# Kernel tuning notes

Hardware: AMD Instinct MI355X
Metric: run time of the kernel (lower is better)

Reference implementation:

```python
import jax, jax.numpy as jnp
import numpy as np

MARGIN = 1.0
EPS = 1e-8  # torch.cosine_similarity default eps


def _cosine(a, b):
    num = jnp.sum(a * b, axis=1)
    den = jnp.maximum(jnp.linalg.norm(a, axis=1) * jnp.linalg.norm(b, axis=1), EPS)
    return num / den


def setup_inputs() -> dict:
    key = jax.random.key(0)
    k1, k2 = jax.random.split(key)
    B, D = 8192, 512
    anchor = jax.random.normal(k1, (B, D), dtype=jnp.float32)
    positive = jax.random.normal(k2, (B, D), dtype=jnp.float32)
    return {"anchor": anchor, "positive": positive}


def reference(anchor, positive):
    B = positive.shape[0]
    a_n = anchor / jnp.linalg.norm(anchor, axis=1, keepdims=True)
    p_n = positive / jnp.linalg.norm(positive, axis=1, keepdims=True)
    sim = a_n @ p_n.T                      # [B, B] cosine similarity
    mask = 1.0 - jnp.eye(B, dtype=sim.dtype)
    sim = sim * mask                       # zero diagonal
    # margin branch of NegariveSampler (margin=1): abs(sim - margin), zeros -> -inf, argmax
    score = jnp.abs(sim - MARGIN) * mask
    score = jnp.where(score == 0.0, -jnp.inf, score)
    neg_idx = jnp.argmax(score, axis=1)    # [B]
    neg = p_n[neg_idx]                     # gather normalized positives as negatives
    cos_ap = _cosine(anchor, positive)
    cos_an = _cosine(anchor, neg)
    loss = jax.nn.relu(MARGIN + cos_ap - cos_an)
    return loss.mean()
```

## Files before the change

kernel.cpp:

```cpp
#include <hip/hip_runtime.h>
#include <stdint.h>

typedef int   i32x8 __attribute__((ext_vector_type(8)));
typedef float f32x4 __attribute__((ext_vector_type(4)));

#define B_ROWS 8192
#define D_DIM  512

__device__ __forceinline__ uint32_t enc_f32(float f) {
  uint32_t s = __float_as_uint(f);
  return (s & 0x80000000u) ? ~s : (s | 0x80000000u);
}
__device__ __forceinline__ float dec_f32(uint32_t e) {
  uint32_t s = (e & 0x80000000u) ? (e ^ 0x80000000u) : ~e;
  return __uint_as_float(s);
}

__global__ __launch_bounds__(256) void norm_kernel(
    const float* __restrict__ anchor, const float* __restrict__ positive,
    uint32_t* __restrict__ a8, uint32_t* __restrict__ p8,
    float* __restrict__ cos_ap, uint32_t* __restrict__ minenc)
{
  const int wave = threadIdx.x >> 6, lane = threadIdx.x & 63;
  const int r = blockIdx.x * 4 + wave;

  const float4* av = (const float4*)(anchor   + (size_t)r * D_DIM) + lane * 2;
  const float4* pv = (const float4*)(positive + (size_t)r * D_DIM) + lane * 2;
  float4 a0 = av[0], a1 = av[1];
  float4 p0 = pv[0], p1 = pv[1];

  float sa = a0.x*a0.x + a0.y*a0.y + a0.z*a0.z + a0.w*a0.w
           + a1.x*a1.x + a1.y*a1.y + a1.z*a1.z + a1.w*a1.w;
  float sp = p0.x*p0.x + p0.y*p0.y + p0.z*p0.z + p0.w*p0.w
           + p1.x*p1.x + p1.y*p1.y + p1.z*p1.z + p1.w*p1.w;
  float dp = a0.x*p0.x + a0.y*p0.y + a0.z*p0.z + a0.w*p0.w
           + a1.x*p1.x + a1.y*p1.y + a1.z*p1.z + a1.w*p1.w;

#pragma unroll
  for (int d = 1; d < 64; d <<= 1) {
    sa += __shfl_xor(sa, d);
    sp += __shfl_xor(sp, d);
    dp += __shfl_xor(dp, d);
  }

  const float na = sqrtf(sa), np = sqrtf(sp);
  const float ia = 1.0f / na, ip = 1.0f / np;

  float na0 = a0.x*ia, na1 = a0.y*ia, na2 = a0.z*ia, na3 = a0.w*ia;
  float na4 = a1.x*ia, na5 = a1.y*ia, na6 = a1.z*ia, na7 = a1.w*ia;
  float np0 = p0.x*ip, np1 = p0.y*ip, np2 = p0.z*ip, np3 = p0.w*ip;
  float np4 = p1.x*ip, np5 = p1.y*ip, np6 = p1.z*ip, np7 = p1.w*ip;

  uint32_t aw0 = __builtin_amdgcn_cvt_pk_fp8_f32(na0, na1, 0,  false);
  aw0          = __builtin_amdgcn_cvt_pk_fp8_f32(na2, na3, aw0, true);
  uint32_t aw1 = __builtin_amdgcn_cvt_pk_fp8_f32(na4, na5, 0,  false);
  aw1          = __builtin_amdgcn_cvt_pk_fp8_f32(na6, na7, aw1, true);
  uint32_t pw0 = __builtin_amdgcn_cvt_pk_fp8_f32(np0, np1, 0,  false);
  pw0          = __builtin_amdgcn_cvt_pk_fp8_f32(np2, np3, pw0, true);
  uint32_t pw1 = __builtin_amdgcn_cvt_pk_fp8_f32(np4, np5, 0,  false);
  pw1          = __builtin_amdgcn_cvt_pk_fp8_f32(np6, np7, pw1, true);

  ((uint2*)a8)[(size_t)r * 64 + lane] = make_uint2(aw0, aw1);
  ((uint2*)p8)[(size_t)r * 64 + lane] = make_uint2(pw0, pw1);

  if (lane == 0) {
    cos_ap[r] = dp / fmaxf(na * np, 1e-8f);
    minenc[r] = 0xFFFFFFFFu;
  }
}

__device__ __forceinline__ void load16_to_lds(const void* g, void* l) {
  __builtin_amdgcn_global_load_lds(
      (__attribute__((address_space(1))) uint32_t*)(uintptr_t)(g),
      (__attribute__((address_space(3))) uint32_t*)(uintptr_t)(l),
      16, 0, 0);
}

__global__ __launch_bounds__(256, 3) void simmin_kernel(
    const uint8_t* __restrict__ a8, const uint8_t* __restrict__ p8,
    uint32_t* __restrict__ minenc)
{
  __shared__ __attribute__((aligned(16))) uint8_t Plds[2][128 * 128];
  __shared__ float redmin[256];

  const int tid  = threadIdx.x;
  const int lane = tid & 63;
  const int wave = tid >> 6;
  const int waveM = wave >> 1, waveN = wave & 1;
  const int quad = lane >> 4;
  const int l15  = lane & 15;

  const int bid = blockIdx.x;
  const int blockRow = (bid & 7) * 8 + ((bid >> 3) & 7);
  const int blockCol = bid >> 6;

  f32x4 acc[4][4];
  const f32x4 zero = {0.f, 0.f, 0.f, 0.f};
#pragma unroll
  for (int i = 0; i < 4; i++)
#pragma unroll
    for (int j = 0; j < 4; j++) acc[i][j] = zero;

  const int srow = lane >> 3;
  const int sk   = (lane & 7) ^ srow;
  const uint8_t* pBase = p8 + (size_t)(blockCol * 128) * D_DIM;

  auto stage = [&](int k0, int buf) {
#pragma unroll
    for (int c = 0; c < 4; c++) {
      const int chunk = wave * 4 + c;
      const size_t goff = (size_t)(chunk * 8 + srow) * D_DIM + k0 + sk * 16;
      load16_to_lds(pBase + goff, &Plds[buf][chunk * 1024]);
    }
  };

  const uint8_t* aFragBase =
      a8 + (size_t)(blockRow * 128 + waveM * 64 + l15) * D_DIM + quad * 32;

  stage(0, 0);

#pragma unroll
  for (int k = 0; k < 4; k++) {
    const int buf = k & 1;
    const int k0  = k * 128;

    i32x8 af[4];
#pragma unroll
    for (int mf = 0; mf < 4; mf++) {
      const uint8_t* ap = aFragBase + (size_t)(mf * 16) * D_DIM + k0;
      const int4 lo = *(const int4*)(ap);
      const int4 hi = *(const int4*)(ap + 16);
      af[mf] = (i32x8){lo.x, lo.y, lo.z, lo.w, hi.x, hi.y, hi.z, hi.w};
    }

    __syncthreads();

    i32x8 bfr[4];
#pragma unroll
    for (int nf = 0; nf < 4; nf++) {
      const int r = waveN * 64 + nf * 16 + l15;
      const int rx = r & 7;
      const int4 lo = *(const int4*)&Plds[buf][r * 128 + (((quad * 2 + 0) ^ rx) * 16)];
      const int4 hi = *(const int4*)&Plds[buf][r * 128 + (((quad * 2 + 1) ^ rx) * 16)];
      bfr[nf] = (i32x8){lo.x, lo.y, lo.z, lo.w, hi.x, hi.y, hi.z, hi.w};
    }

    if (k < 3) stage(k0 + 128, buf ^ 1);

#pragma unroll
    for (int mf = 0; mf < 4; mf++)
#pragma unroll
      for (int nf = 0; nf < 4; nf++)
        acc[mf][nf] = __builtin_amdgcn_mfma_scale_f32_16x16x128_f8f6f4(
            af[mf], bfr[nf], acc[mf][nf],
            0, 0,
            0, 0x7F7F7F7F,
            0, 0x7F7F7F7F);
  }

  const int rowTileBase = blockRow * 128 + waveM * 64;
  const int colTileBase = blockCol * 128 + waveN * 64;

  float rm[4][4];
#pragma unroll
  for (int mf = 0; mf < 4; mf++)
#pragma unroll
    for (int r = 0; r < 4; r++) rm[mf][r] = 3.0e38f;

#pragma unroll
  for (int mf = 0; mf < 4; mf++) {
#pragma unroll
    for (int nf = 0; nf < 4; nf++) {
      const int col = colTileBase + nf * 16 + l15;
#pragma unroll
      for (int r = 0; r < 4; r++) {
        const int row = rowTileBase + mf * 16 + quad * 4 + r;
        const float v = acc[mf][nf][r];
        rm[mf][r] = (row == col) ? rm[mf][r] : fminf(rm[mf][r], v);
      }
    }
  }
#pragma unroll
  for (int d = 1; d < 16; d <<= 1)
#pragma unroll
    for (int mf = 0; mf < 4; mf++)
#pragma unroll
      for (int r = 0; r < 4; r++)
        rm[mf][r] = fminf(rm[mf][r], __shfl_xor(rm[mf][r], d));

  if (l15 == 0) {
#pragma unroll
    for (int mf = 0; mf < 4; mf++)
#pragma unroll
      for (int r = 0; r < 4; r++)
        redmin[waveN * 128 + waveM * 64 + mf * 16 + quad * 4 + r] = rm[mf][r];
  }
  __syncthreads();

  if (tid < 128) {
    const float m = fminf(redmin[tid], redmin[128 + tid]);
    atomicMin(&minenc[blockRow * 128 + tid], enc_f32(m));
  }
}

__global__ __launch_bounds__(1024) void finalize_kernel(
    const uint32_t* __restrict__ minenc, const float* __restrict__ cos_ap,
    float* __restrict__ out)
{
  float sum = 0.0f;
#pragma unroll
  for (int r = threadIdx.x; r < B_ROWS; r += 1024)
    sum += fmaxf(0.0f, 1.0f + cos_ap[r] - dec_f32(minenc[r]));

#pragma unroll
  for (int d = 1; d < 64; d <<= 1) sum += __shfl_xor(sum, d);
  __shared__ float s[16];
  if ((threadIdx.x & 63) == 0) s[threadIdx.x >> 6] = sum;
  __syncthreads();
  if (threadIdx.x < 64) {
    float t = (threadIdx.x < 16) ? s[threadIdx.x] : 0.0f;
#pragma unroll
    for (int d = 1; d < 16; d <<= 1) t += __shfl_xor(t, d);
    if (threadIdx.x == 0) out[0] = t * (1.0f / (float)B_ROWS);
  }
}

extern "C" void kernel_launch(void* const* d_in, const int* in_sizes, int n_in,
                              void* d_out, int out_size, void* d_ws, size_t ws_size,
                              hipStream_t stream) {
  const float* anchor   = (const float*)d_in[0];
  const float* positive = (const float*)d_in[1];

  char* ws = (char*)d_ws;
  uint32_t* a8     = (uint32_t*)(ws);
  uint32_t* p8     = (uint32_t*)(ws + (4ull << 20));
  float*    cos_ap = (float*)(ws + (8ull << 20));
  uint32_t* minenc = (uint32_t*)(ws + (8ull << 20) + (32ull << 10));
  float*    out = (float*)d_out;

  norm_kernel<<<B_ROWS / 4, 256, 0, stream>>>(anchor, positive, a8, p8,
                                              cos_ap, minenc);
  simmin_kernel<<<4096, 256, 0, stream>>>((const uint8_t*)a8,
                                          (const uint8_t*)p8, minenc);
  finalize_kernel<<<1, 1024, 0, stream>>>(minenc, cos_ap, out);
}
```

Before: 152.2 us.

## Fuse finalize reduction into simmin via last-block counter, preload A fragments

Removes the separate finalize kernel launch by having the last simmin block to finish (found with an atomic done counter reset in norm_kernel) run the loss reduction. All four K-slices of A fragments are now loaded into registers up front instead of once per iteration, and launch bounds drop from 3 to 2 blocks per SM so the larger register footprint fits. The aim is to save one launch plus its gap and to hide global load latency, at the cost of occupancy and an extra atomic and fence in every block.

```diff
diff --git a/kernel.cpp b/kernel.cpp
--- a/kernel.cpp
+++ b/kernel.cpp
@@ -6,6 +6,7 @@
 
 #define B_ROWS 8192
 #define D_DIM  512
+#define N_BLOCKS 4096
 
 __device__ __forceinline__ uint32_t enc_f32(float f) {
   uint32_t s = __float_as_uint(f);
@@ -19,10 +20,13 @@
 __global__ __launch_bounds__(256) void norm_kernel(
     const float* __restrict__ anchor, const float* __restrict__ positive,
     uint32_t* __restrict__ a8, uint32_t* __restrict__ p8,
-    float* __restrict__ cos_ap, uint32_t* __restrict__ minenc)
+    float* __restrict__ cos_ap, uint32_t* __restrict__ minenc,
+    uint32_t* __restrict__ donecnt)
 {
   const int wave = threadIdx.x >> 6, lane = threadIdx.x & 63;
   const int r = blockIdx.x * 4 + wave;
+
+  if (blockIdx.x == 0 && threadIdx.x == 0) *donecnt = 0u;
 
   const float4* av = (const float4*)(anchor   + (size_t)r * D_DIM) + lane * 2;
   const float4* pv = (const float4*)(positive + (size_t)r * D_DIM) + lane * 2;
@@ -76,9 +80,10 @@
       16, 0, 0);
 }
 
-__global__ __launch_bounds__(256, 3) void simmin_kernel(
+__global__ __launch_bounds__(256, 2) void simmin_kernel(
     const uint8_t* __restrict__ a8, const uint8_t* __restrict__ p8,
-    uint32_t* __restrict__ minenc)
+    uint32_t* __restrict__ minenc, const float* __restrict__ cos_ap,
+    uint32_t* __restrict__ donecnt, float* __restrict__ out)
 {
   __shared__ __attribute__((aligned(16))) uint8_t Plds[2][128 * 128];
   __shared__ float redmin[256];
@@ -117,21 +122,23 @@
   const uint8_t* aFragBase =
       a8 + (size_t)(blockRow * 128 + waveM * 64 + l15) * D_DIM + quad * 32;
 
+  i32x8 afk[4][4];
+#pragma unroll
+  for (int k = 0; k < 4; k++) {
+#pragma unroll
+    for (int mf = 0; mf < 4; mf++) {
+      const uint8_t* ap = aFragBase + (size_t)(mf * 16) * D_DIM + k * 128;
+      const int4 lo = *(const int4*)(ap);
+      const int4 hi = *(const int4*)(ap + 16);
+      afk[k][mf] = (i32x8){lo.x, lo.y, lo.z, lo.w, hi.x, hi.y, hi.z, hi.w};
+    }
+  }
+
   stage(0, 0);
 
 #pragma unroll
   for (int k = 0; k < 4; k++) {
     const int buf = k & 1;
-    const int k0  = k * 128;
-
-    i32x8 af[4];
-#pragma unroll
-    for (int mf = 0; mf < 4; mf++) {
-      const uint8_t* ap = aFragBase + (size_t)(mf * 16) * D_DIM + k0;
-      const int4 lo = *(const int4*)(ap);
-      const int4 hi = *(const int4*)(ap + 16);
-      af[mf] = (i32x8){lo.x, lo.y, lo.z, lo.w, hi.x, hi.y, hi.z, hi.w};
-    }
 
     __syncthreads();
 
@@ -145,14 +152,14 @@
       bfr[nf] = (i32x8){lo.x, lo.y, lo.z, lo.w, hi.x, hi.y, hi.z, hi.w};
     }
 
-    if (k < 3) stage(k0 + 128, buf ^ 1);
+    if (k < 3) stage((k + 1) * 128, buf ^ 1);
 
 #pragma unroll
     for (int mf = 0; mf < 4; mf++)
 #pragma unroll
       for (int nf = 0; nf < 4; nf++)
         acc[mf][nf] = __builtin_amdgcn_mfma_scale_f32_16x16x128_f8f6f4(
-            af[mf], bfr[nf], acc[mf][nf],
+            afk[k][mf], bfr[nf], acc[mf][nf],
             0, 0,
             0, 0x7F7F7F7F,
             0, 0x7F7F7F7F);
@@ -201,27 +208,33 @@
     const float m = fminf(redmin[tid], redmin[128 + tid]);
     atomicMin(&minenc[blockRow * 128 + tid], enc_f32(m));
   }
-}
-
-__global__ __launch_bounds__(1024) void finalize_kernel(
-    const uint32_t* __restrict__ minenc, const float* __restrict__ cos_ap,
-    float* __restrict__ out)
-{
+
+  __threadfence();
+  __syncthreads();
+  __shared__ int lastFlag;
+  if (tid == 0) {
+    uint32_t prev = __hip_atomic_fetch_add(donecnt, 1u, __ATOMIC_ACQ_REL,
+                                           __HIP_MEMORY_SCOPE_AGENT);
+    lastFlag = (prev == N_BLOCKS - 1);
+  }
+  __syncthreads();
+  if (!lastFlag) return;
+
   float sum = 0.0f;
 #pragma unroll
-  for (int r = threadIdx.x; r < B_ROWS; r += 1024)
-    sum += fmaxf(0.0f, 1.0f + cos_ap[r] - dec_f32(minenc[r]));
-
+  for (int i = 0; i < B_ROWS / 256; i++) {
+    const int r = i * 256 + tid;
+    const uint32_t e = __hip_atomic_load(&minenc[r], __ATOMIC_RELAXED,
+                                         __HIP_MEMORY_SCOPE_AGENT);
+    sum += fmaxf(0.0f, 1.0f + cos_ap[r] - dec_f32(e));
+  }
 #pragma unroll
   for (int d = 1; d < 64; d <<= 1) sum += __shfl_xor(sum, d);
-  __shared__ float s[16];
-  if ((threadIdx.x & 63) == 0) s[threadIdx.x >> 6] = sum;
-  __syncthreads();
-  if (threadIdx.x < 64) {
-    float t = (threadIdx.x < 16) ? s[threadIdx.x] : 0.0f;
-#pragma unroll
-    for (int d = 1; d < 16; d <<= 1) t += __shfl_xor(t, d);
-    if (threadIdx.x == 0) out[0] = t * (1.0f / (float)B_ROWS);
+  if (lane == 0) redmin[wave] = sum;
+  __syncthreads();
+  if (tid == 0) {
+    const float t = redmin[0] + redmin[1] + redmin[2] + redmin[3];
+    out[0] = t * (1.0f / (float)B_ROWS);
   }
 }
 
@@ -232,15 +245,16 @@
   const float* positive = (const float*)d_in[1];
 
   char* ws = (char*)d_ws;
-  uint32_t* a8     = (uint32_t*)(ws);
-  uint32_t* p8     = (uint32_t*)(ws + (4ull << 20));
-  float*    cos_ap = (float*)(ws + (8ull << 20));
-  uint32_t* minenc = (uint32_t*)(ws + (8ull << 20) + (32ull << 10));
+  uint32_t* a8      = (uint32_t*)(ws);
+  uint32_t* p8      = (uint32_t*)(ws + (4ull << 20));
+  float*    cos_ap  = (float*)(ws + (8ull << 20));
+  uint32_t* minenc  = (uint32_t*)(ws + (8ull << 20) + (32ull << 10));
+  uint32_t* donecnt = (uint32_t*)(ws + (8ull << 20) + (64ull << 10));
   float*    out = (float*)d_out;
 
   norm_kernel<<<B_ROWS / 4, 256, 0, stream>>>(anchor, positive, a8, p8,
-                                              cos_ap, minenc);
-  simmin_kernel<<<4096, 256, 0, stream>>>((const uint8_t*)a8,
-                                          (const uint8_t*)p8, minenc);
-  finalize_kernel<<<1, 1024, 0, stream>>>(minenc, cos_ap, out);
-}
+                                              cos_ap, minenc, donecnt);
+  simmin_kernel<<<N_BLOCKS, 256, 0, stream>>>((const uint8_t*)a8,
+                                              (const uint8_t*)p8, minenc,
+                                              cos_ap, donecnt, out);
+}
```

New measurement: 453.8 us. 198% more time.
